# Kernel optimization log

Hardware: AMD Instinct MI355X
Metric: run time of the kernel (lower is better)

## Reference

```python
import jax, jax.numpy as jnp
import numpy as np

HID = 64  # hidden_dim


def _w(k, shape, fan):
    # torch default: U(-1/sqrt(hidden), 1/sqrt(hidden))
    bound = 1.0 / np.sqrt(fan)
    return jax.random.uniform(k, shape, jnp.float32, -bound, bound)


def setup_inputs() -> dict:
    key = jax.random.key(0)
    ks = jax.random.split(key, 16)
    B, L, S, D = 32, 168, 512, 1
    H = HID
    return {
        "x_seq": jax.random.normal(ks[0], (B, L, S, D), jnp.float32),
        # encoder LSTM layer 0 (input_size=D)
        "W_ih0": _w(ks[1], (4 * H, D), H), "W_hh0": _w(ks[2], (4 * H, H), H),
        "b_ih0": _w(ks[3], (4 * H,), H), "b_hh0": _w(ks[4], (4 * H,), H),
        # encoder LSTM layer 1 (input_size=H)
        "W_ih1": _w(ks[5], (4 * H, H), H), "W_hh1": _w(ks[6], (4 * H, H), H),
        "b_ih1": _w(ks[7], (4 * H,), H), "b_hh1": _w(ks[8], (4 * H,), H),
        # decoder LSTMCell (input_size=D)
        "Wc_ih": _w(ks[9], (4 * H, D), H), "Wc_hh": _w(ks[10], (4 * H, H), H),
        "bc_ih": _w(ks[11], (4 * H,), H), "bc_hh": _w(ks[12], (4 * H,), H),
        # output projection hidden -> input_dim
        "W_out": _w(ks[13], (D, H), H), "b_out": _w(ks[14], (D,), H),
        "horizon": 24,
    }


def _cell(x, h, c, Wih, Whh, bih, bhh):
    # torch gate order: i, f, g, o
    g = x @ Wih.T + bih + h @ Whh.T + bhh  # (N, 4H)
    i, f, gg, o = jnp.split(g, 4, axis=-1)
    c = jax.nn.sigmoid(f) * c + jax.nn.sigmoid(i) * jnp.tanh(gg)
    h = jax.nn.sigmoid(o) * jnp.tanh(c)
    return h, c


def _lstm_layer(x, Wih, Whh, bih, bhh):
    # x: (N, L, D_in) -> outputs (N, L, H), final h, c
    N = x.shape[0]
    Hd = Whh.shape[1]
    init = (jnp.zeros((N, Hd), x.dtype), jnp.zeros((N, Hd), x.dtype))

    def step(carry, xt):
        h, c = carry
        h, c = _cell(xt, h, c, Wih, Whh, bih, bhh)
        return (h, c), h

    (h, c), ys = jax.lax.scan(step, init, jnp.swapaxes(x, 0, 1))
    return jnp.swapaxes(ys, 0, 1), h, c


def reference(x_seq, W_ih0, W_hh0, b_ih0, b_hh0, W_ih1, W_hh1, b_ih1, b_hh1,
              Wc_ih, Wc_hh, bc_ih, bc_hh, W_out, b_out, horizon):
    B, L, S, D = x_seq.shape
    # (B, L, S, D) -> (B*S, L, D)
    x = jnp.transpose(x_seq, (0, 2, 1, 3)).reshape(B * S, L, D)
    # 2-layer encoder LSTM; dropout is identity in eval mode
    y1, _, _ = _lstm_layer(x, W_ih0, W_hh0, b_ih0, b_hh0)
    _, h, c = _lstm_layer(y1, W_ih1, W_hh1, b_ih1, b_hh1)
    x_cur = x[:, -1, :]

    def dec(carry, _):
        h, c, xc = carry
        h, c = _cell(xc, h, c, Wc_ih, Wc_hh, bc_ih, bc_hh)
        y = h @ W_out.T + b_out  # (N, D)
        return (h, c, y), y

    _, ys = jax.lax.scan(dec, (h, c, x_cur), None, length=horizon)  # (Hor, N, D)
    y = jnp.transpose(ys, (1, 0, 2)).reshape(B, S, horizon, D)
    return jnp.transpose(y, (0, 2, 1, 3))  # (B, Hor, S, D)
```

## Files before the change

### kernel.cpp

```cpp
#include <hip/hip_runtime.h>

typedef __attribute__((ext_vector_type(8))) short short8;
typedef __attribute__((ext_vector_type(4))) float f32x4;

#define MFMA16(a, b, c) __builtin_amdgcn_mfma_f32_16x16x32_bf16((a), (b), (c), 0, 0, 0)

constexpr int Bv  = 32;
constexpr int Lv  = 168;
constexpr int Sv  = 512;
constexpr int HZv = 24;
constexpr int Mv  = 64;
constexpr int HSTR = 88;
constexpr int HBUF = Mv * HSTR;
constexpr int WFR  = 512;
constexpr int WMAT = 32 * WFR;

__device__ __forceinline__ float b2f(short s) {
    unsigned u = ((unsigned)(unsigned short)s) << 16;
    return __builtin_bit_cast(float, u);
}
__device__ __forceinline__ short f2b(float f) {
    unsigned u = __builtin_bit_cast(unsigned, f);
    unsigned r = (u + 0x7FFFu + ((u >> 16) & 1u)) >> 16;
    return (short)(unsigned short)r;
}
__device__ __forceinline__ float sigm(float x) {
    float e = __builtin_amdgcn_exp2f(-1.44269504088896f * x);
    return __builtin_amdgcn_rcpf(1.0f + e);
}
__device__ __forceinline__ float tanh_(float x) {
    float e = __builtin_amdgcn_exp2f(2.88539008177793f * x);
    return 1.0f - 2.0f * __builtin_amdgcn_rcpf(e + 1.0f);
}
__device__ __forceinline__ void hi8(const float* __restrict__ p, short8& hi) {
#pragma unroll
    for (int j = 0; j < 8; ++j) hi[j] = f2b(p[j]);
}

__global__ __launch_bounds__(1024)
void sitewise_lstm(const float* __restrict__ x_seq,
                   const float* __restrict__ Wih0, const float* __restrict__ Whh0,
                   const float* __restrict__ bih0, const float* __restrict__ bhh0,
                   const float* __restrict__ Wih1, const float* __restrict__ Whh1,
                   const float* __restrict__ bih1, const float* __restrict__ bhh1,
                   const float* __restrict__ Wcih, const float* __restrict__ Wchh,
                   const float* __restrict__ bcih, const float* __restrict__ bchh,
                   const float* __restrict__ Wout, const float* __restrict__ bout,
                   float* __restrict__ out)
{
    __shared__ __align__(16) short Wlds[3 * WMAT];
    __shared__ __align__(16) short Hhi[4 * HBUF];
    __shared__ float woutF[64];
    __shared__ float ybufF[Mv];

    const int tid  = threadIdx.x;
    const int wv   = tid >> 6;
    const int lane = tid & 63;
    const int q    = lane >> 4;
    const int col  = lane & 15;
    const int mh   = wv >> 2;
    const int U    = wv & 3;
    const int bid  = blockIdx.x;
    const int b    = bid >> 3;
    const int s0   = (bid & 7) << 6;
    const int uu   = U * 16 + col;
    const int me   = mh * 16 + q * 4;

    const int roA  = (mh * 16 + col) * HSTR + q * 8;
    const int wiA  = me * HSTR + uu;
    const int wb0  = (U * 8) * WFR + lane * 8;
    const int wb1  = WMAT + wb0;
    const int wb2  = 2 * WMAT + wb0;

    for (int i = tid; i < 4 * HBUF / 2; i += 1024) ((int*)Hhi)[i] = 0;
    if (tid < 64) woutF[tid] = Wout[tid];

    for (int idx = tid; idx < 96 * 64; idx += 1024) {
        const int fid = idx >> 6;
        const int ln  = idx & 63;
        const int mat = fid >> 5;
        const int fm  = fid & 31;
        const int Uw  = fm >> 3;
        const int kc  = (fm >> 2) & 1;
        const int g   = fm & 3;
        const float* Wm = (mat == 0) ? Whh0 : (mat == 1) ? Wih1 : Whh1;
        const int j   = g * 64 + Uw * 16 + (ln & 15);
        const int cc  = kc * 32 + (ln >> 4) * 8;
        short8 hv; hi8(Wm + j * 64 + cc, hv);
        *(short8*)(Wlds + fid * WFR + ln * 8) = hv;
    }

    const float* xbF = x_seq + b * Lv * Sv + s0;

    float bias0[4], bias1[4], wih0gE[4];
#pragma unroll
    for (int g = 0; g < 4; ++g) {
        const int j = g * 64 + uu;
        bias0[g]  = bih0[j] + bhh0[j];
        bias1[g]  = bih1[j] + bhh1[j];
        wih0gE[g] = Wih0[j];
    }

    float c0[4], c1[4];
#pragma unroll
    for (int i = 0; i < 4; ++i) { c0[i] = 0.f; c1[i] = 0.f; }

    __syncthreads();

#define ENC_STEP(T, B0P, B0N, B1P, B1N) do {                                          \
        f32x4 xv = *(const f32x4*)(xbF + (T) * Sv + me);                              \
        short8 ah0 = *(const short8*)(Hhi + (B0P) + roA);                             \
        short8 ah1 = *(const short8*)(Hhi + (B0P) + roA + 32);                        \
        short8 wf[8];                                                                 \
        _Pragma("unroll")                                                             \
        for (int f = 0; f < 8; ++f) wf[f] = *(const short8*)(Wlds + wb0 + f * WFR);   \
        f32x4 pre0[4];                                                                \
        _Pragma("unroll")                                                             \
        for (int g = 0; g < 4; ++g)                                                   \
            pre0[g] = (f32x4){bias0[g], bias0[g], bias0[g], bias0[g]};                \
        _Pragma("unroll")                                                             \
        for (int g = 0; g < 4; ++g) pre0[g] = MFMA16(ah0, wf[g],     pre0[g]);        \
        _Pragma("unroll")                                                             \
        for (int g = 0; g < 4; ++g) pre0[g] = MFMA16(ah1, wf[4 + g], pre0[g]);        \
        _Pragma("unroll")                                                             \
        for (int r = 0; r < 4; ++r) {                                                 \
            const float xw = xv[r];                                                   \
            const float ig = sigm (pre0[0][r] + xw * wih0gE[0]);                      \
            const float fg = sigm (pre0[1][r] + xw * wih0gE[1]);                      \
            const float gt = tanh_(pre0[2][r] + xw * wih0gE[2]);                      \
            const float og = sigm (pre0[3][r] + xw * wih0gE[3]);                      \
            const float c  = fg * c0[r] + ig * gt;                                    \
            c0[r] = c;                                                                \
            Hhi[(B0N) + wiA + r * HSTR] = f2b(og * tanh_(c));                         \
        }                                                                             \
        __syncthreads();                       \
        short8 bh0 = *(const short8*)(Hhi + (B0N) + roA);                             \
        short8 bh1 = *(const short8*)(Hhi + (B0N) + roA + 32);                        \
        short8 dh0 = *(const short8*)(Hhi + (B1P) + roA);                             \
        short8 dh1 = *(const short8*)(Hhi + (B1P) + roA + 32);                        \
        f32x4 pre1[4];                                                                \
        _Pragma("unroll")                                                             \
        for (int g = 0; g < 4; ++g)                                                   \
            pre1[g] = (f32x4){bias1[g], bias1[g], bias1[g], bias1[g]};                \
        _Pragma("unroll")                                                             \
        for (int f = 0; f < 8; ++f) wf[f] = *(const short8*)(Wlds + wb1 + f * WFR);   \
        _Pragma("unroll")                                                             \
        for (int g = 0; g < 4; ++g) pre1[g] = MFMA16(bh0, wf[g],     pre1[g]);        \
        _Pragma("unroll")                                                             \
        for (int g = 0; g < 4; ++g) pre1[g] = MFMA16(bh1, wf[4 + g], pre1[g]);        \
        _Pragma("unroll")                                                             \
        for (int f = 0; f < 8; ++f) wf[f] = *(const short8*)(Wlds + wb2 + f * WFR);   \
        _Pragma("unroll")                                                             \
        for (int g = 0; g < 4; ++g) pre1[g] = MFMA16(dh0, wf[g],     pre1[g]);        \
        _Pragma("unroll")                                                             \
        for (int g = 0; g < 4; ++g) pre1[g] = MFMA16(dh1, wf[4 + g], pre1[g]);        \
        _Pragma("unroll")                                                             \
        for (int r = 0; r < 4; ++r) {                                                 \
            const float ig = sigm (pre1[0][r]);                                       \
            const float fg = sigm (pre1[1][r]);                                       \
            const float gt = tanh_(pre1[2][r]);                                       \
            const float og = sigm (pre1[3][r]);                                       \
            const float c  = fg * c1[r] + ig * gt;                                    \
            c1[r] = c;                                                                \
            Hhi[(B1N) + wiA + r * HSTR] = f2b(og * tanh_(c));                         \
        }                                                                             \
             \
             \
    } while (0)

    for (int t = 0; t < Lv; t += 2) {
        ENC_STEP(t,     0 * HBUF, 1 * HBUF, 2 * HBUF, 3 * HBUF);
        ENC_STEP(t + 1, 1 * HBUF, 0 * HBUF, 3 * HBUF, 2 * HBUF);
    }
#undef ENC_STEP

    for (int idx = tid; idx < 32 * 64; idx += 1024) {
        const int fid = idx >> 6;
        const int ln  = idx & 63;
        const int Uw  = fid >> 3;
        const int kc  = (fid >> 2) & 1;
        const int g   = fid & 3;
        const int j   = g * 64 + Uw * 16 + (ln & 15);
        const int cc  = kc * 32 + (ln >> 4) * 8;
        short8 hv; hi8(Wchh + j * 64 + cc, hv);
        *(short8*)(Wlds + fid * WFR + ln * 8) = hv;
    }
    float biasc[4], wcihgE[4];
#pragma unroll
    for (int g = 0; g < 4; ++g) {
        const int j = g * 64 + uu;
        biasc[g]  = bcih[j] + bchh[j];
        wcihgE[g] = Wcih[j];
    }
    if (tid < Mv) ybufF[tid] = xbF[(Lv - 1) * Sv + tid];
    __syncthreads();

    const float boutF = bout[0];
    float* outp = out + b * HZv * Sv + s0;

#define DEC_STEP(T, B1P, B1N) do {                                                    \
        short8 ah0 = *(const short8*)(Hhi + (B1P) + roA);                             \
        short8 ah1 = *(const short8*)(Hhi + (B1P) + roA + 32);                        \
        short8 wf[8];                                                                 \
        _Pragma("unroll")                                                             \
        for (int f = 0; f < 8; ++f) wf[f] = *(const short8*)(Wlds + wb0 + f * WFR);   \
        float yv[4];                                                                  \
        _Pragma("unroll")                                                             \
        for (int r = 0; r < 4; ++r)                                                   \
            yv[r] = ybufF[me + r];                                                    \
        f32x4 prc[4];                                                                 \
        _Pragma("unroll")                                                             \
        for (int g = 0; g < 4; ++g)                                                   \
            prc[g] = (f32x4){biasc[g], biasc[g], biasc[g], biasc[g]};                 \
        _Pragma("unroll")                                                             \
        for (int g = 0; g < 4; ++g) prc[g] = MFMA16(ah0, wf[g],     prc[g]);          \
        _Pragma("unroll")                                                             \
        for (int g = 0; g < 4; ++g) prc[g] = MFMA16(ah1, wf[4 + g], prc[g]);          \
        _Pragma("unroll")                                                             \
        for (int r = 0; r < 4; ++r) {                                                 \
            const float xw = yv[r];                                                   \
            const float ig = sigm (prc[0][r] + xw * wcihgE[0]);                       \
            const float fg = sigm (prc[1][r] + xw * wcihgE[1]);                       \
            const float gt = tanh_(prc[2][r] + xw * wcihgE[2]);                       \
            const float og = sigm (prc[3][r] + xw * wcihgE[3]);                       \
            const float c  = fg * c1[r] + ig * gt;                                    \
            c1[r] = c;                                                                \
            Hhi[(B1N) + wiA + r * HSTR] = f2b(og * tanh_(c));                         \
        }                                                                             \
        __syncthreads();                         \
        {                             \
            const int m  = tid >> 4;                                                  \
            const int pp = tid & 15;                                                  \
            float s = 0.f;                                                            \
            _Pragma("unroll")                                                         \
            for (int k = 0; k < 4; ++k)                                               \
                s += b2f(Hhi[(B1N) + m * HSTR + pp * 4 + k]) * woutF[pp * 4 + k];     \
            s += __shfl_xor(s, 1, 64);                                                \
            s += __shfl_xor(s, 2, 64);                                                \
            s += __shfl_xor(s, 4, 64);                                                \
            s += __shfl_xor(s, 8, 64);                                                \
            if (pp == 0) {                                                            \
                const float y = s + boutF;                                            \
                outp[(T) * Sv + m] = y;                                               \
                ybufF[m] = y;                                                         \
            }                                                                         \
        }                                                                             \
        __syncthreads();                             \
    } while (0)

    for (int t = 0; t < HZv; t += 2) {
        DEC_STEP(t,     2 * HBUF, 3 * HBUF);
        DEC_STEP(t + 1, 3 * HBUF, 2 * HBUF);
    }
#undef DEC_STEP
}

extern "C" void kernel_launch(void* const* d_in, const int* in_sizes, int n_in,
                              void* d_out, int out_size, void* d_ws, size_t ws_size,
                              hipStream_t stream)
{
    const float* x_seq = (const float*)d_in[0];
    const float* Wih0  = (const float*)d_in[1];
    const float* Whh0  = (const float*)d_in[2];
    const float* bih0  = (const float*)d_in[3];
    const float* bhh0  = (const float*)d_in[4];
    const float* Wih1  = (const float*)d_in[5];
    const float* Whh1  = (const float*)d_in[6];
    const float* bih1  = (const float*)d_in[7];
    const float* bhh1  = (const float*)d_in[8];
    const float* Wcih  = (const float*)d_in[9];
    const float* Wchh  = (const float*)d_in[10];
    const float* bcih  = (const float*)d_in[11];
    const float* bchh  = (const float*)d_in[12];
    const float* Wout  = (const float*)d_in[13];
    const float* bout  = (const float*)d_in[14];
    float* out = (float*)d_out;

    hipLaunchKernelGGL(sitewise_lstm, dim3(Bv * (Sv / Mv)), dim3(1024), 0, stream,
                       x_seq, Wih0, Whh0, bih0, bhh0, Wih1, Whh1, bih1, bhh1,
                       Wcih, Wchh, bcih, bchh, Wout, bout, out);
}
```

Before: 505.9 us.

## Wavefront-pipeline LSTM layers across warp groups with register-resident weights

```diff
diff --git a/kernel.cpp b/kernel.cpp
--- a/kernel.cpp
+++ b/kernel.cpp
@@ -13,7 +13,9 @@
 constexpr int HSTR = 88;
 constexpr int HBUF = Mv * HSTR;
 constexpr int WFR  = 512;
-constexpr int WMAT = 32 * WFR;
+
+__device__ __constant__ float GF[4] = {-1.44269504088896f, -1.44269504088896f,
+                                        2.88539008177793f, -1.44269504088896f};
 
 __device__ __forceinline__ float b2f(short s) {
     unsigned u = ((unsigned)(unsigned short)s) << 16;
@@ -24,17 +26,26 @@
     unsigned r = (u + 0x7FFFu + ((u >> 16) & 1u)) >> 16;
     return (short)(unsigned short)r;
 }
-__device__ __forceinline__ float sigm(float x) {
-    float e = __builtin_amdgcn_exp2f(-1.44269504088896f * x);
+__device__ __forceinline__ unsigned pkbf16(float lo, float hi) {
+    unsigned r;
+    asm("v_cvt_pk_bf16_f32 %0, %1, %2" : "=v"(r) : "v"(lo), "v"(hi));
+    return r;
+}
+__device__ __forceinline__ float sigmP(float p) {
+    float e = __builtin_amdgcn_exp2f(p);
     return __builtin_amdgcn_rcpf(1.0f + e);
+}
+__device__ __forceinline__ float tanhP(float p) {
+    float e = __builtin_amdgcn_exp2f(p);
+    return 1.0f - 2.0f * __builtin_amdgcn_rcpf(e + 1.0f);
 }
 __device__ __forceinline__ float tanh_(float x) {
     float e = __builtin_amdgcn_exp2f(2.88539008177793f * x);
     return 1.0f - 2.0f * __builtin_amdgcn_rcpf(e + 1.0f);
 }
-__device__ __forceinline__ void hi8(const float* __restrict__ p, short8& hi) {
-#pragma unroll
-    for (int j = 0; j < 8; ++j) hi[j] = f2b(p[j]);
+__device__ __forceinline__ void hi8s(const float* __restrict__ p, float s, short8& hi) {
+#pragma unroll
+    for (int j = 0; j < 8; ++j) hi[j] = f2b(p[j] * s);
 }
 
 __global__ __launch_bounds__(1024)
@@ -48,7 +59,7 @@
                    const float* __restrict__ Wout, const float* __restrict__ bout,
                    float* __restrict__ out)
 {
-    __shared__ __align__(16) short Wlds[3 * WMAT];
+    __shared__ __align__(16) short Wlds[32 * WFR];
     __shared__ __align__(16) short Hhi[4 * HBUF];
     __shared__ float woutF[64];
     __shared__ float ybufF[Mv];
@@ -58,121 +69,22 @@
     const int lane = tid & 63;
     const int q    = lane >> 4;
     const int col  = lane & 15;
-    const int mh   = wv >> 2;
-    const int U    = wv & 3;
+    const bool isL0 = (wv < 8);
+    const int wq   = wv & 7;
+    const int mh   = wq >> 2;
+    const int U    = wq & 3;
     const int bid  = blockIdx.x;
     const int b    = bid >> 3;
     const int s0   = (bid & 7) << 6;
     const int uu   = U * 16 + col;
-    const int me   = mh * 16 + q * 4;
-
-    const int roA  = (mh * 16 + col) * HSTR + q * 8;
+    const int me   = mh * 32 + q * 4;
+
+    const int roA  = (mh * 32 + col) * HSTR + q * 8;
     const int wiA  = me * HSTR + uu;
-    const int wb0  = (U * 8) * WFR + lane * 8;
-    const int wb1  = WMAT + wb0;
-    const int wb2  = 2 * WMAT + wb0;
+    const int wb   = (U * 8) * WFR + lane * 8;
 
     for (int i = tid; i < 4 * HBUF / 2; i += 1024) ((int*)Hhi)[i] = 0;
     if (tid < 64) woutF[tid] = Wout[tid];
-
-    for (int idx = tid; idx < 96 * 64; idx += 1024) {
-        const int fid = idx >> 6;
-        const int ln  = idx & 63;
-        const int mat = fid >> 5;
-        const int fm  = fid & 31;
-        const int Uw  = fm >> 3;
-        const int kc  = (fm >> 2) & 1;
-        const int g   = fm & 3;
-        const float* Wm = (mat == 0) ? Whh0 : (mat == 1) ? Wih1 : Whh1;
-        const int j   = g * 64 + Uw * 16 + (ln & 15);
-        const int cc  = kc * 32 + (ln >> 4) * 8;
-        short8 hv; hi8(Wm + j * 64 + cc, hv);
-        *(short8*)(Wlds + fid * WFR + ln * 8) = hv;
-    }
-
-    const float* xbF = x_seq + b * Lv * Sv + s0;
-
-    float bias0[4], bias1[4], wih0gE[4];
-#pragma unroll
-    for (int g = 0; g < 4; ++g) {
-        const int j = g * 64 + uu;
-        bias0[g]  = bih0[j] + bhh0[j];
-        bias1[g]  = bih1[j] + bhh1[j];
-        wih0gE[g] = Wih0[j];
-    }
-
-    float c0[4], c1[4];
-#pragma unroll
-    for (int i = 0; i < 4; ++i) { c0[i] = 0.f; c1[i] = 0.f; }
-
-    __syncthreads();
-
-#define ENC_STEP(T, B0P, B0N, B1P, B1N) do {                                          \
-        f32x4 xv = *(const f32x4*)(xbF + (T) * Sv + me);                              \
-        short8 ah0 = *(const short8*)(Hhi + (B0P) + roA);                             \
-        short8 ah1 = *(const short8*)(Hhi + (B0P) + roA + 32);                        \
-        short8 wf[8];                                                                 \
-        _Pragma("unroll")                                                             \
-        for (int f = 0; f < 8; ++f) wf[f] = *(const short8*)(Wlds + wb0 + f * WFR);   \
-        f32x4 pre0[4];                                                                \
-        _Pragma("unroll")                                                             \
-        for (int g = 0; g < 4; ++g)                                                   \
-            pre0[g] = (f32x4){bias0[g], bias0[g], bias0[g], bias0[g]};                \
-        _Pragma("unroll")                                                             \
-        for (int g = 0; g < 4; ++g) pre0[g] = MFMA16(ah0, wf[g],     pre0[g]);        \
-        _Pragma("unroll")                                                             \
-        for (int g = 0; g < 4; ++g) pre0[g] = MFMA16(ah1, wf[4 + g], pre0[g]);        \
-        _Pragma("unroll")                                                             \
-        for (int r = 0; r < 4; ++r) {                                                 \
-            const float xw = xv[r];                                                   \
-            const float ig = sigm (pre0[0][r] + xw * wih0gE[0]);                      \
-            const float fg = sigm (pre0[1][r] + xw * wih0gE[1]);                      \
-            const float gt = tanh_(pre0[2][r] + xw * wih0gE[2]);                      \
-            const float og = sigm (pre0[3][r] + xw * wih0gE[3]);                      \
-            const float c  = fg * c0[r] + ig * gt;                                    \
-            c0[r] = c;                                                                \
-            Hhi[(B0N) + wiA + r * HSTR] = f2b(og * tanh_(c));                         \
-        }                                                                             \
-        __syncthreads();                       \
-        short8 bh0 = *(const short8*)(Hhi + (B0N) + roA);                             \
-        short8 bh1 = *(const short8*)(Hhi + (B0N) + roA + 32);                        \
-        short8 dh0 = *(const short8*)(Hhi + (B1P) + roA);                             \
-        short8 dh1 = *(const short8*)(Hhi + (B1P) + roA + 32);                        \
-        f32x4 pre1[4];                                                                \
-        _Pragma("unroll")                                                             \
-        for (int g = 0; g < 4; ++g)                                                   \
-            pre1[g] = (f32x4){bias1[g], bias1[g], bias1[g], bias1[g]};                \
-        _Pragma("unroll")                                                             \
-        for (int f = 0; f < 8; ++f) wf[f] = *(const short8*)(Wlds + wb1 + f * WFR);   \
-        _Pragma("unroll")                                                             \
-        for (int g = 0; g < 4; ++g) pre1[g] = MFMA16(bh0, wf[g],     pre1[g]);        \
-        _Pragma("unroll")                                                             \
-        for (int g = 0; g < 4; ++g) pre1[g] = MFMA16(bh1, wf[4 + g], pre1[g]);        \
-        _Pragma("unroll")                                                             \
-        for (int f = 0; f < 8; ++f) wf[f] = *(const short8*)(Wlds + wb2 + f * WFR);   \
-        _Pragma("unroll")                                                             \
-        for (int g = 0; g < 4; ++g) pre1[g] = MFMA16(dh0, wf[g],     pre1[g]);        \
-        _Pragma("unroll")                                                             \
-        for (int g = 0; g < 4; ++g) pre1[g] = MFMA16(dh1, wf[4 + g], pre1[g]);        \
-        _Pragma("unroll")                                                             \
-        for (int r = 0; r < 4; ++r) {                                                 \
-            const float ig = sigm (pre1[0][r]);                                       \
-            const float fg = sigm (pre1[1][r]);                                       \
-            const float gt = tanh_(pre1[2][r]);                                       \
-            const float og = sigm (pre1[3][r]);                                       \
-            const float c  = fg * c1[r] + ig * gt;                                    \
-            c1[r] = c;                                                                \
-            Hhi[(B1N) + wiA + r * HSTR] = f2b(og * tanh_(c));                         \
-        }                                                                             \
-             \
-             \
-    } while (0)
-
-    for (int t = 0; t < Lv; t += 2) {
-        ENC_STEP(t,     0 * HBUF, 1 * HBUF, 2 * HBUF, 3 * HBUF);
-        ENC_STEP(t + 1, 1 * HBUF, 0 * HBUF, 3 * HBUF, 2 * HBUF);
-    }
-#undef ENC_STEP
 
     for (int idx = tid; idx < 32 * 64; idx += 1024) {
         const int fid = idx >> 6;
@@ -182,15 +94,130 @@
         const int g   = fid & 3;
         const int j   = g * 64 + Uw * 16 + (ln & 15);
         const int cc  = kc * 32 + (ln >> 4) * 8;
-        short8 hv; hi8(Wchh + j * 64 + cc, hv);
+        short8 hv; hi8s(Whh1 + j * 64 + cc, GF[g], hv);
         *(short8*)(Wlds + fid * WFR + ln * 8) = hv;
     }
-    float biasc[4], wcihgE[4];
+
+    const float* xbF = x_seq + b * Lv * Sv + s0;
+
+    float ba[4], we[4];
+    short8 wreg[8];
+    const float* WmA = isL0 ? Whh0 : Wih1;
 #pragma unroll
     for (int g = 0; g < 4; ++g) {
         const int j = g * 64 + uu;
-        biasc[g]  = bcih[j] + bchh[j];
-        wcihgE[g] = Wcih[j];
+        ba[g] = (isL0 ? (bih0[j] + bhh0[j]) : (bih1[j] + bhh1[j])) * GF[g];
+        we[g] = Wih0[j] * GF[g];
+#pragma unroll
+        for (int kc = 0; kc < 2; ++kc)
+            hi8s(WmA + j * 64 + kc * 32 + q * 8, GF[g], wreg[kc * 4 + g]);
+    }
+
+    float cs[8];
+#pragma unroll
+    for (int i = 0; i < 8; ++i) cs[i] = 0.f;
+
+    __syncthreads();
+
+#define L0BODY(T, RP, WP) do {                                                        \
+        _Pragma("unroll")                                                             \
+        for (int mt = 0; mt < 2; ++mt) {                                              \
+            const f32x4 xv = *(const f32x4*)(xbF + (T) * Sv + me + mt * 16);          \
+            const short8 a0 = *(const short8*)(Hhi + (RP) * HBUF + roA + mt * 16 * HSTR);      \
+            const short8 a1 = *(const short8*)(Hhi + (RP) * HBUF + roA + mt * 16 * HSTR + 32); \
+            f32x4 pre[4];                                                             \
+            _Pragma("unroll")                                                         \
+            for (int g = 0; g < 4; ++g) pre[g] = (f32x4){ba[g], ba[g], ba[g], ba[g]}; \
+            _Pragma("unroll")                                                         \
+            for (int g = 0; g < 4; ++g) pre[g] = MFMA16(a0, wreg[g],     pre[g]);     \
+            _Pragma("unroll")                                                         \
+            for (int g = 0; g < 4; ++g) pre[g] = MFMA16(a1, wreg[4 + g], pre[g]);     \
+            float hv[4];                                                              \
+            _Pragma("unroll")                                                         \
+            for (int r = 0; r < 4; ++r) {                                             \
+                const float xw = xv[r];                                               \
+                const float ig = sigmP(pre[0][r] + xw * we[0]);                       \
+                const float fg = sigmP(pre[1][r] + xw * we[1]);                       \
+                const float gt = tanhP(pre[2][r] + xw * we[2]);                       \
+                const float og = sigmP(pre[3][r] + xw * we[3]);                       \
+                const float c  = fg * cs[mt * 4 + r] + ig * gt;                       \
+                cs[mt * 4 + r] = c;                                                   \
+                hv[r] = og * tanh_(c);                                                \
+            }                                                                         \
+            const unsigned p01 = pkbf16(hv[0], hv[1]);                                \
+            const unsigned p23 = pkbf16(hv[2], hv[3]);                                \
+            Hhi[(WP) * HBUF + wiA + (mt * 16 + 0) * HSTR] = (short)p01;               \
+            Hhi[(WP) * HBUF + wiA + (mt * 16 + 1) * HSTR] = (short)(p01 >> 16);       \
+            Hhi[(WP) * HBUF + wiA + (mt * 16 + 2) * HSTR] = (short)p23;               \
+            Hhi[(WP) * HBUF + wiA + (mt * 16 + 3) * HSTR] = (short)(p23 >> 16);       \
+        }                                                                             \
+    } while (0)
+
+#define L1BODY(RP0, RPH, WPH) do {                                                    \
+        _Pragma("unroll")                                                             \
+        for (int mt = 0; mt < 2; ++mt) {                                              \
+            const short8 b0 = *(const short8*)(Hhi + (RP0) * HBUF + roA + mt * 16 * HSTR);      \
+            const short8 b1 = *(const short8*)(Hhi + (RP0) * HBUF + roA + mt * 16 * HSTR + 32); \
+            const short8 d0 = *(const short8*)(Hhi + (RPH) * HBUF + roA + mt * 16 * HSTR);      \
+            const short8 d1 = *(const short8*)(Hhi + (RPH) * HBUF + roA + mt * 16 * HSTR + 32); \
+            f32x4 pre[4];                                                             \
+            _Pragma("unroll")                                                         \
+            for (int g = 0; g < 4; ++g) pre[g] = (f32x4){ba[g], ba[g], ba[g], ba[g]}; \
+            _Pragma("unroll")                                                         \
+            for (int g = 0; g < 4; ++g) pre[g] = MFMA16(b0, wreg[g],     pre[g]);     \
+            _Pragma("unroll")                                                         \
+            for (int g = 0; g < 4; ++g) pre[g] = MFMA16(b1, wreg[4 + g], pre[g]);     \
+            _Pragma("unroll")                                                         \
+            for (int g = 0; g < 4; ++g) {                                             \
+                const short8 wf = *(const short8*)(Wlds + wb + g * WFR);              \
+                pre[g] = MFMA16(d0, wf, pre[g]);                                      \
+            }                                                                         \
+            _Pragma("unroll")                                                         \
+            for (int g = 0; g < 4; ++g) {                                             \
+                const short8 wf = *(const short8*)(Wlds + wb + (4 + g) * WFR);        \
+                pre[g] = MFMA16(d1, wf, pre[g]);                                      \
+            }                                                                         \
+            float hv[4];                                                              \
+            _Pragma("unroll")                                                         \
+            for (int r = 0; r < 4; ++r) {                                             \
+                const float ig = sigmP(pre[0][r]);                                    \
+                const float fg = sigmP(pre[1][r]);                                    \
+                const float gt = tanhP(pre[2][r]);                                    \
+                const float og = sigmP(pre[3][r]);                                    \
+                const float c  = fg * cs[mt * 4 + r] + ig * gt;                       \
+                cs[mt * 4 + r] = c;                                                   \
+                hv[r] = og * tanh_(c);                                                \
+            }                                                                         \
+            const unsigned p01 = pkbf16(hv[0], hv[1]);                                \
+            const unsigned p23 = pkbf16(hv[2], hv[3]);                                \
+            Hhi[(WPH) * HBUF + wiA + (mt * 16 + 0) * HSTR] = (short)p01;              \
+            Hhi[(WPH) * HBUF + wiA + (mt * 16 + 1) * HSTR] = (short)(p01 >> 16);      \
+            Hhi[(WPH) * HBUF + wiA + (mt * 16 + 2) * HSTR] = (short)p23;              \
+            Hhi[(WPH) * HBUF + wiA + (mt * 16 + 3) * HSTR] = (short)(p23 >> 16);      \
+        }                                                                             \
+    } while (0)
+
+    if (isL0) L0BODY(0, 1, 0);
+    __syncthreads();
+    for (int k = 1; k < 167; k += 2) {
+        if (isL0) L0BODY(k, 0, 1); else L1BODY(0, 3, 2);
+        __syncthreads();
+        if (isL0) L0BODY(k + 1, 1, 0); else L1BODY(1, 2, 3);
+        __syncthreads();
+    }
+    if (isL0) L0BODY(167, 0, 1); else L1BODY(0, 3, 2);
+    __syncthreads();
+    if (!isL0) L1BODY(1, 2, 3);
+    __syncthreads();
+
+#pragma unroll
+    for (int g = 0; g < 4; ++g) {
+        const int j = g * 64 + uu;
+        ba[g] = (bcih[j] + bchh[j]) * GF[g];
+        we[g] = Wcih[j] * GF[g];
+#pragma unroll
+        for (int kc = 0; kc < 2; ++kc)
+            hi8s(Wchh + j * 64 + kc * 32 + q * 8, GF[g], wreg[kc * 4 + g]);
     }
     if (tid < Mv) ybufF[tid] = xbF[(Lv - 1) * Sv + tid];
     __syncthreads();
@@ -198,34 +225,39 @@
     const float boutF = bout[0];
     float* outp = out + b * HZv * Sv + s0;
 
-#define DEC_STEP(T, B1P, B1N) do {                                                    \
-        short8 ah0 = *(const short8*)(Hhi + (B1P) + roA);                             \
-        short8 ah1 = *(const short8*)(Hhi + (B1P) + roA + 32);                        \
-        short8 wf[8];                                                                 \
-        _Pragma("unroll")                                                             \
-        for (int f = 0; f < 8; ++f) wf[f] = *(const short8*)(Wlds + wb0 + f * WFR);   \
-        float yv[4];                                                                  \
-        _Pragma("unroll")                                                             \
-        for (int r = 0; r < 4; ++r)                                                   \
-            yv[r] = ybufF[me + r];                                                    \
-        f32x4 prc[4];                                                                 \
-        _Pragma("unroll")                                                             \
-        for (int g = 0; g < 4; ++g)                                                   \
-            prc[g] = (f32x4){biasc[g], biasc[g], biasc[g], biasc[g]};                 \
-        _Pragma("unroll")                                                             \
-        for (int g = 0; g < 4; ++g) prc[g] = MFMA16(ah0, wf[g],     prc[g]);          \
-        _Pragma("unroll")                                                             \
-        for (int g = 0; g < 4; ++g) prc[g] = MFMA16(ah1, wf[4 + g], prc[g]);          \
-        _Pragma("unroll")                                                             \
-        for (int r = 0; r < 4; ++r) {                                                 \
-            const float xw = yv[r];                                                   \
-            const float ig = sigm (prc[0][r] + xw * wcihgE[0]);                       \
-            const float fg = sigm (prc[1][r] + xw * wcihgE[1]);                       \
-            const float gt = tanh_(prc[2][r] + xw * wcihgE[2]);                       \
-            const float og = sigm (prc[3][r] + xw * wcihgE[3]);                       \
-            const float c  = fg * c1[r] + ig * gt;                                    \
-            c1[r] = c;                                                                \
-            Hhi[(B1N) + wiA + r * HSTR] = f2b(og * tanh_(c));                         \
+#define DECBODY(T, RPH, WPH) do {                                                     \
+        if (!isL0) {                                                                  \
+            _Pragma("unroll")                                                         \
+            for (int mt = 0; mt < 2; ++mt) {                                          \
+                const f32x4 yv = *(const f32x4*)(ybufF + me + mt * 16);               \
+                const short8 a0 = *(const short8*)(Hhi + (RPH) * HBUF + roA + mt * 16 * HSTR);      \
+                const short8 a1 = *(const short8*)(Hhi + (RPH) * HBUF + roA + mt * 16 * HSTR + 32); \
+                f32x4 pre[4];                                                         \
+                _Pragma("unroll")                                                     \
+                for (int g = 0; g < 4; ++g) pre[g] = (f32x4){ba[g], ba[g], ba[g], ba[g]}; \
+                _Pragma("unroll")                                                     \
+                for (int g = 0; g < 4; ++g) pre[g] = MFMA16(a0, wreg[g],     pre[g]); \
+                _Pragma("unroll")                                                     \
+                for (int g = 0; g < 4; ++g) pre[g] = MFMA16(a1, wreg[4 + g], pre[g]); \
+                float hv[4];                                                          \
+                _Pragma("unroll")                                                     \
+                for (int r = 0; r < 4; ++r) {                                         \
+                    const float xw = yv[r];                                           \
+                    const float ig = sigmP(pre[0][r] + xw * we[0]);                   \
+                    const float fg = sigmP(pre[1][r] + xw * we[1]);                   \
+                    const float gt = tanhP(pre[2][r] + xw * we[2]);                   \
+                    const float og = sigmP(pre[3][r] + xw * we[3]);                   \
+                    const float c  = fg * cs[mt * 4 + r] + ig * gt;                   \
+                    cs[mt * 4 + r] = c;                                               \
+                    hv[r] = og * tanh_(c);                                            \
+                }                                                                     \
+                const unsigned p01 = pkbf16(hv[0], hv[1]);                            \
+                const unsigned p23 = pkbf16(hv[2], hv[3]);                            \
+                Hhi[(WPH) * HBUF + wiA + (mt * 16 + 0) * HSTR] = (short)p01;          \
+                Hhi[(WPH) * HBUF + wiA + (mt * 16 + 1) * HSTR] = (short)(p01 >> 16);  \
+                Hhi[(WPH) * HBUF + wiA + (mt * 16 + 2) * HSTR] = (short)p23;          \
+                Hhi[(WPH) * HBUF + wiA + (mt * 16 + 3) * HSTR] = (short)(p23 >> 16);  \
+            }                                                                         \
         }                                                                             \
         __syncthreads();                         \
         {                             \
@@ -233,8 +265,8 @@
             const int pp = tid & 15;                                                  \
             float s = 0.f;                                                            \
             _Pragma("unroll")                                                         \
-            for (int k = 0; k < 4; ++k)                                               \
-                s += b2f(Hhi[(B1N) + m * HSTR + pp * 4 + k]) * woutF[pp * 4 + k];     \
+            for (int k2 = 0; k2 < 4; ++k2)                                            \
+                s += b2f(Hhi[(WPH) * HBUF + m * HSTR + pp * 4 + k2]) * woutF[pp * 4 + k2]; \
             s += __shfl_xor(s, 1, 64);                                                \
             s += __shfl_xor(s, 2, 64);                                                \
             s += __shfl_xor(s, 4, 64);                                                \
@@ -249,10 +281,12 @@
     } while (0)
 
     for (int t = 0; t < HZv; t += 2) {
-        DEC_STEP(t,     2 * HBUF, 3 * HBUF);
-        DEC_STEP(t + 1, 3 * HBUF, 2 * HBUF);
-    }
-#undef DEC_STEP
+        DECBODY(t,     3, 2);
+        DECBODY(t + 1, 2, 3);
+    }
+#undef DECBODY
+#undef L1BODY
+#undef L0BODY
 }
 
 extern "C" void kernel_launch(void* const* d_in, const int* in_sizes, int n_in,
```

Result: faster. 465.9 us (-7.9%).
